# Optimization experiments

Measured on AMD Instinct MI355X. Metric: run time of the kernel, lower is better.

Reference implementation:

```python
import jax, jax.numpy as jnp
import numpy as np

B, H, W, C = 32, 56, 56, 512
WS, SHIFT, NH = 7, 3, 16
HID = 4 * C
EPS = 1e-5


def layernorm(x, g, b):
    m = jnp.mean(x, axis=-1, keepdims=True)
    v = jnp.mean(jnp.square(x - m), axis=-1, keepdims=True)
    return (x - m) * jax.lax.rsqrt(v + EPS) * g + b


def setup_inputs() -> dict:
    key = jax.random.key(0)
    ks = jax.random.split(key, 16)
    s = 0.02
    return {
        "x": jax.random.normal(ks[0], (B, H * W, C), jnp.float32),
        "wqkv": jax.random.normal(ks[1], (3 * C, C), jnp.float32) * s,
        "bqkv": jnp.zeros((3 * C,), jnp.float32),
        "wo": jax.random.normal(ks[2], (C, C), jnp.float32) * s,
        "bo": jnp.zeros((C,), jnp.float32),
        "g1": jnp.ones((C,), jnp.float32),
        "b1": jnp.zeros((C,), jnp.float32),
        "g2": jnp.ones((C,), jnp.float32),
        "b2": jnp.zeros((C,), jnp.float32),
        "w_mlp1": jax.random.normal(ks[3], (HID, C), jnp.float32) * s,
        "b_mlp1": jnp.zeros((HID,), jnp.float32),
        "w_mlp2": jax.random.normal(ks[4], (C, HID), jnp.float32) * s,
        "b_mlp2": jnp.zeros((C,), jnp.float32),
    }


def window_partition(x4):
    # (B,H,W,C) -> (B*nW, WS*WS, C)
    x = x4.reshape(B, H // WS, WS, W // WS, WS, C)
    return x.transpose(0, 1, 3, 2, 4, 5).reshape(-1, WS * WS, C)


def window_reverse(win):
    # (B*nW, WS*WS, C) -> (B,H,W,C)
    x = win.reshape(B, H // WS, W // WS, WS, WS, C)
    return x.transpose(0, 1, 3, 2, 4, 5).reshape(B, H, W, C)


def mha(xn, wqkv, bqkv, wo, bo):
    NW, T, _ = xn.shape
    Dh = C // NH
    qkv = xn @ wqkv.T + bqkv                      # (NW, T, 3C)
    q, k, v = jnp.split(qkv, 3, axis=-1)
    sh = lambda t: t.reshape(NW, T, NH, Dh).transpose(0, 2, 1, 3)  # (NW,NH,T,Dh)
    q, k, v = sh(q), sh(k), sh(v)
    scores = jnp.einsum('whqd,whkd->whqk', q, k) * (Dh ** -0.5)
    a = jax.nn.softmax(scores, axis=-1)
    o = jnp.einsum('whqk,whkd->whqd', a, v).transpose(0, 2, 1, 3).reshape(NW, T, C)
    return o @ wo.T + bo


def reference(x, wqkv, bqkv, wo, bo, g1, b1, g2, b2, w_mlp1, b_mlp1, w_mlp2, b_mlp2):
    x4 = x.reshape(B, H, W, C)
    shifted = jnp.roll(x4, (-SHIFT, -SHIFT), axis=(1, 2))
    win = window_partition(shifted)               # (B*64, 49, C)
    shortcut = win
    wn = layernorm(win, g1, b1)
    attn = mha(wn, wqkv, bqkv, wo, bo)
    win = shortcut + attn
    _ = window_reverse(win)  # NOTE: discarded, faithfully matching the source (x is rebuilt from shifted_x)
    xr = jnp.roll(shifted, (SHIFT, SHIFT), axis=(1, 2)).reshape(B, H * W, C)
    h = layernorm(xr, g2, b2)
    h = jax.nn.gelu(h @ w_mlp1.T + b_mlp1, approximate=False) @ w_mlp2.T + b_mlp2
    return xr + h
```

## Files before the change

kernel.cpp:

```cpp
#include <hip/hip_runtime.h>
#include <hip/hip_bf16.h>
#include <cstdint>
#include <cstddef>

#define MROWS 100352
#define CDIM  512
#define HDIM  2048

typedef __attribute__((ext_vector_type(8))) short   short8;
typedef __attribute__((ext_vector_type(8))) __bf16  bf16x8;
typedef __attribute__((ext_vector_type(4))) __bf16  bf16x4;
typedef __attribute__((ext_vector_type(4))) float   floatx4;

static __device__ __forceinline__ unsigned short f2bf(float f) {
  union { float f; unsigned int u; } c; c.f = f;
  unsigned int u = c.u;
  return (unsigned short)((u + 0x7FFFu + ((u >> 16) & 1u)) >> 16);
}

static __device__ __forceinline__ void gload_lds16(const void* g, void* l) {
  __builtin_amdgcn_global_load_lds(
      (const __attribute__((address_space(1))) void*)g,
      (__attribute__((address_space(3))) void*)l, 16, 0, 0);
}

#define BAR()   asm volatile("s_barrier" ::: "memory")
#define LGKM0() asm volatile("s_waitcnt lgkmcnt(0)" ::: "memory")
#define VMC0()  asm volatile("s_waitcnt vmcnt(0)" ::: "memory")

__global__ void cast_weights(const float4* __restrict__ s1, unsigned short* __restrict__ d1,
                             const float4* __restrict__ s2, unsigned short* __restrict__ d2) {
  int t = blockIdx.x * 256 + threadIdx.x;
  const int N4 = (HDIM * CDIM) / 4;
  const float4* s; unsigned short* d; int idx;
  if (t < N4) { s = s1; d = d1; idx = t; }
  else        { s = s2; d = d2; idx = t - N4; }
  float4 f = s[idx];
  ushort4 u = make_ushort4(f2bf(f.x), f2bf(f.y), f2bf(f.z), f2bf(f.w));
  *reinterpret_cast<ushort4*>(d + (size_t)idx * 4) = u;
}

__global__ void ln_cast(const float* __restrict__ x, const float* __restrict__ g,
                        const float* __restrict__ b, unsigned short* __restrict__ xn) {
  const int row  = blockIdx.x * 4 + (threadIdx.x >> 6);
  const int lane = threadIdx.x & 63;
  const float4* xr = reinterpret_cast<const float4*>(x + (size_t)row * CDIM);
  const float4 v0 = xr[lane], v1 = xr[lane + 64];
  float s  = v0.x + v0.y + v0.z + v0.w + v1.x + v1.y + v1.z + v1.w;
  float ss = v0.x*v0.x + v0.y*v0.y + v0.z*v0.z + v0.w*v0.w
           + v1.x*v1.x + v1.y*v1.y + v1.z*v1.z + v1.w*v1.w;
#pragma unroll
  for (int o = 1; o < 64; o <<= 1) { s += __shfl_xor(s, o); ss += __shfl_xor(ss, o); }
  const float mean = s * (1.0f / CDIM);
  const float rstd = rsqrtf(ss * (1.0f / CDIM) - mean * mean + 1e-5f);
  const float4* g4 = reinterpret_cast<const float4*>(g);
  const float4* b4 = reinterpret_cast<const float4*>(b);
  const float4 ga = g4[lane], gb = g4[lane + 64];
  const float4 ba = b4[lane], bb = b4[lane + 64];
  ushort4 o0 = make_ushort4(
      f2bf((v0.x - mean) * rstd * ga.x + ba.x),
      f2bf((v0.y - mean) * rstd * ga.y + ba.y),
      f2bf((v0.z - mean) * rstd * ga.z + ba.z),
      f2bf((v0.w - mean) * rstd * ga.w + ba.w));
  ushort4 o1 = make_ushort4(
      f2bf((v1.x - mean) * rstd * gb.x + bb.x),
      f2bf((v1.y - mean) * rstd * gb.y + bb.y),
      f2bf((v1.z - mean) * rstd * gb.z + bb.z),
      f2bf((v1.w - mean) * rstd * gb.w + bb.w));
  unsigned short* orow = xn + (size_t)row * CDIM;
  *reinterpret_cast<ushort4*>(orow + lane * 4)        = o0;
  *reinterpret_cast<ushort4*>(orow + (lane + 64) * 4) = o1;
}

template<int KDIM, int NDIM, int EPI>
__global__ __launch_bounds__(256, 4) void gemm_m97(
    const unsigned short* __restrict__ A, const unsigned short* __restrict__ Bw,
    const float* __restrict__ bias, const float* __restrict__ resid,
    void* __restrict__ Cout) {
  constexpr int nt = KDIM / 32;
  __shared__ __align__(16) unsigned short smA[128 * 32];
  __shared__ __align__(16) unsigned short smB[128 * 32];

  const int tid  = threadIdx.x;
  const int lane = tid & 63, w = tid >> 6;
  const int swr = w >> 1, swc = w & 1;
  const int frow = lane & 15, fslot = lane >> 4;

  constexpr int GX = NDIM / 128;
  const int nwg = gridDim.x;
  const int lid = ((int)blockIdx.x & 7) * (nwg >> 3) + ((int)blockIdx.x >> 3);
  const int m0 = (lid / GX) * 128, n0 = (lid % GX) * 128;

  const size_t ldb = (size_t)KDIM * 2;
  const int srow = tid >> 2;
  const int scb  = ((tid ^ (tid >> 3)) & 3) * 16;
  const char* gA = (const char*)A  + (size_t)(m0 + srow) * ldb + scb;
  const char* gB = (const char*)Bw + (size_t)(n0 + srow) * ldb + scb;

  auto STG = [&](int kt) {
    const char* sa = gA + (size_t)kt * 64;
    const char* sb = gB + (size_t)kt * 64;
    gload_lds16(sa,            &smA[tid * 8]);
    gload_lds16(sa + 64 * ldb, &smA[2048 + tid * 8]);
    gload_lds16(sb,            &smB[tid * 8]);
    gload_lds16(sb + 64 * ldb, &smB[2048 + tid * 8]);
  };

  floatx4 acc[4][4] = {};

  STG(0);
  VMC0();
  BAR();

  for (int kt = 0; kt < nt; ++kt) {
    bf16x8 a[4], b[4];
#pragma unroll
    for (int mi = 0; mi < 4; ++mi) {
      const int row = swr * 64 + mi * 16 + frow;
      const int sl  = fslot ^ ((row >> 1) & 3);
      a[mi] = __builtin_bit_cast(bf16x8,
          *reinterpret_cast<const short8*>(&smA[row * 32 + sl * 8]));
    }
#pragma unroll
    for (int nj = 0; nj < 4; ++nj) {
      const int row = swc * 64 + nj * 16 + frow;
      const int sl  = fslot ^ ((row >> 1) & 3);
      b[nj] = __builtin_bit_cast(bf16x8,
          *reinterpret_cast<const short8*>(&smB[row * 32 + sl * 8]));
    }

    LGKM0();
    BAR();
    if (kt + 1 < nt) STG(kt + 1);

    __builtin_amdgcn_s_setprio(1);
#pragma unroll
    for (int mi = 0; mi < 4; ++mi)
#pragma unroll
      for (int nj = 0; nj < 4; ++nj)
        acc[mi][nj] = __builtin_amdgcn_mfma_f32_16x16x32_bf16(
            b[nj], a[mi], acc[mi][nj], 0, 0, 0);
    __builtin_amdgcn_s_setprio(0);

    if (kt + 1 < nt) { VMC0(); BAR(); }
  }

  const int em = lane & 15;
  const int en = fslot << 2;

  float4 bj[4];
#pragma unroll
  for (int nj = 0; nj < 4; ++nj)
    bj[nj] = *reinterpret_cast<const float4*>(&bias[n0 + swc * 64 + nj * 16 + en]);

#pragma unroll
  for (int mi = 0; mi < 4; ++mi) {
    const int gm = m0 + swr * 64 + mi * 16 + em;
    const size_t rowoff = (size_t)gm * NDIM + n0 + swc * 64 + en;
#pragma unroll
    for (int nj = 0; nj < 4; ++nj) {
      const float4 bb = bj[nj];
      const floatx4 av = acc[mi][nj];
      float v0 = av[0] + bb.x, v1 = av[1] + bb.y;
      float v2 = av[2] + bb.z, v3 = av[3] + bb.w;
      const size_t off = rowoff + nj * 16;
      if (EPI == 1) {
        v0 *= __builtin_amdgcn_rcpf(1.0f + __expf(-1.702f * v0));
        v1 *= __builtin_amdgcn_rcpf(1.0f + __expf(-1.702f * v1));
        v2 *= __builtin_amdgcn_rcpf(1.0f + __expf(-1.702f * v2));
        v3 *= __builtin_amdgcn_rcpf(1.0f + __expf(-1.702f * v3));
        bf16x4 o = { (__bf16)v0, (__bf16)v1, (__bf16)v2, (__bf16)v3 };
        *reinterpret_cast<bf16x4*>((unsigned short*)Cout + off) = o;
      } else {
        const float4 r4 = *reinterpret_cast<const float4*>(resid + off);
        float4 o = make_float4(v0 + r4.x, v1 + r4.y, v2 + r4.z, v3 + r4.w);
        *reinterpret_cast<float4*>((float*)Cout + off) = o;
      }
    }
  }
}

extern "C" void kernel_launch(void* const* d_in, const int* in_sizes, int n_in,
                              void* d_out, int out_size, void* d_ws, size_t ws_size,
                              hipStream_t stream) {
  const float* x   = (const float*)d_in[0];
  const float* g2  = (const float*)d_in[7];
  const float* b2  = (const float*)d_in[8];
  const float* w1  = (const float*)d_in[9];
  const float* b1  = (const float*)d_in[10];
  const float* w2  = (const float*)d_in[11];
  const float* b2m = (const float*)d_in[12];
  float* out = (float*)d_out;


  unsigned short* w1b = (unsigned short*)d_ws;
  unsigned short* w2b = w1b + (size_t)HDIM * CDIM;
  unsigned short* G   = w2b + (size_t)HDIM * CDIM;
  unsigned short* xn = (unsigned short*)d_out;

  cast_weights<<<2048, 256, 0, stream>>>((const float4*)w1, w1b, (const float4*)w2, w2b);
  ln_cast<<<MROWS / 4, 256, 0, stream>>>(x, g2, b2, xn);

  gemm_m97<CDIM, HDIM, 1>
      <<<dim3((MROWS / 128) * (HDIM / 128)), 256, 0, stream>>>(
          xn, w1b, b1, nullptr, (void*)G);

  gemm_m97<HDIM, CDIM, 2>
      <<<dim3((MROWS / 128) * (CDIM / 128)), 256, 0, stream>>>(
          G, w2b, b2m, x, (void*)out);
}
```

Before: 685.5 us.

## Double-buffer LDS tiles in GEMM to prefetch two k-steps ahead

Turns the single LDS A/B tile into a two-slot ring. Loads for step kt+2 are issued while step kt computes, and the wait becomes vmcnt(4), so one stage of global-to-LDS loads can stay in flight. This is meant to hide global load latency that the old wait-all-then-barrier schedule exposed each iteration. LDS use per block doubles to 32KB, which may reduce how many blocks fit per CU alongside the launch bound of 4.

```diff
diff --git a/kernel.cpp b/kernel.cpp
--- a/kernel.cpp
+++ b/kernel.cpp
@@ -26,6 +26,7 @@
 
 #define BAR()   asm volatile("s_barrier" ::: "memory")
 #define LGKM0() asm volatile("s_waitcnt lgkmcnt(0)" ::: "memory")
+#define VMC4()  asm volatile("s_waitcnt vmcnt(4)" ::: "memory")
 #define VMC0()  asm volatile("s_waitcnt vmcnt(0)" ::: "memory")
 
 __global__ void cast_weights(const float4* __restrict__ s1, unsigned short* __restrict__ d1,
@@ -78,8 +79,8 @@
     const float* __restrict__ bias, const float* __restrict__ resid,
     void* __restrict__ Cout) {
   constexpr int nt = KDIM / 32;
-  __shared__ __align__(16) unsigned short smA[128 * 32];
-  __shared__ __align__(16) unsigned short smB[128 * 32];
+  __shared__ __align__(16) unsigned short smA[2][128 * 32];
+  __shared__ __align__(16) unsigned short smB[2][128 * 32];
 
   const int tid  = threadIdx.x;
   const int lane = tid & 63, w = tid >> 6;
@@ -97,41 +98,43 @@
   const char* gA = (const char*)A  + (size_t)(m0 + srow) * ldb + scb;
   const char* gB = (const char*)Bw + (size_t)(n0 + srow) * ldb + scb;
 
-  auto STG = [&](int kt) {
+  auto STG = [&](int kt, int buf) {
     const char* sa = gA + (size_t)kt * 64;
     const char* sb = gB + (size_t)kt * 64;
-    gload_lds16(sa,            &smA[tid * 8]);
-    gload_lds16(sa + 64 * ldb, &smA[2048 + tid * 8]);
-    gload_lds16(sb,            &smB[tid * 8]);
-    gload_lds16(sb + 64 * ldb, &smB[2048 + tid * 8]);
+    gload_lds16(sa,            &smA[buf][tid * 8]);
+    gload_lds16(sa + 64 * ldb, &smA[buf][2048 + tid * 8]);
+    gload_lds16(sb,            &smB[buf][tid * 8]);
+    gload_lds16(sb + 64 * ldb, &smB[buf][2048 + tid * 8]);
   };
 
   floatx4 acc[4][4] = {};
 
-  STG(0);
-  VMC0();
+  STG(0, 0);
+  STG(1, 1);
+  VMC4();
   BAR();
 
   for (int kt = 0; kt < nt; ++kt) {
+    const int p = kt & 1;
     bf16x8 a[4], b[4];
 #pragma unroll
     for (int mi = 0; mi < 4; ++mi) {
       const int row = swr * 64 + mi * 16 + frow;
       const int sl  = fslot ^ ((row >> 1) & 3);
       a[mi] = __builtin_bit_cast(bf16x8,
-          *reinterpret_cast<const short8*>(&smA[row * 32 + sl * 8]));
+          *reinterpret_cast<const short8*>(&smA[p][row * 32 + sl * 8]));
     }
 #pragma unroll
     for (int nj = 0; nj < 4; ++nj) {
       const int row = swc * 64 + nj * 16 + frow;
       const int sl  = fslot ^ ((row >> 1) & 3);
       b[nj] = __builtin_bit_cast(bf16x8,
-          *reinterpret_cast<const short8*>(&smB[row * 32 + sl * 8]));
+          *reinterpret_cast<const short8*>(&smB[p][row * 32 + sl * 8]));
     }
 
     LGKM0();
     BAR();
-    if (kt + 1 < nt) STG(kt + 1);
+    if (kt + 2 < nt) STG(kt + 2, p);
 
     __builtin_amdgcn_s_setprio(1);
 #pragma unroll
@@ -142,7 +145,8 @@
             b[nj], a[mi], acc[mi][nj], 0, 0, 0);
     __builtin_amdgcn_s_setprio(0);
 
-    if (kt + 1 < nt) { VMC0(); BAR(); }
+    if (kt + 2 < nt)      { VMC4(); BAR(); }
+    else if (kt + 1 < nt) { VMC0(); BAR(); }
   }
 
   const int em = lane & 15;
```

After: 687.2 us. No clear change (+0.2%).
